# Kernel tuning notes

Measured on AMD Instinct MI355X. Metric: run time of the kernel, lower is better.

## Reference

```python
import jax, jax.numpy as jnp
import numpy as np

B, C, H, W = 16, 256, 64, 64
K = 3


def _binary_act(x):
    # forward: sign(x); backward: piecewise-polynomial STE surrogate out3
    sg = jax.lax.stop_gradient
    f32 = x.dtype
    m1 = (x < -1).astype(f32)
    m2 = (x < 0).astype(f32)
    m3 = (x < 1).astype(f32)
    out1 = -1.0 * m1 + (x * x + 2.0 * x) * (1.0 - m1)
    out2 = out1 * m2 + (-x * x + 2.0 * x) * (1.0 - m2)
    out3 = out2 * m3 + 1.0 * (1.0 - m3)
    return sg(jnp.sign(x)) - sg(out3) + out3


def _binarize_weight(w):
    # per-output-channel scale * sign(w) in forward; clipped identity STE in backward
    sg = jax.lax.stop_gradient
    scale = sg(jnp.mean(jnp.abs(w), axis=(1, 2, 3), keepdims=True))  # (O,1,1,1)
    bw_no_grad = scale * jnp.sign(w)
    cw = jnp.clip(w, -1.0, 1.0)
    return sg(bw_no_grad) - sg(cw) + cw


def setup_inputs() -> dict:
    key = jax.random.key(0)
    k1, k2 = jax.random.split(key, 2)
    x = jax.random.normal(k1, (B, C, H, W), dtype=jnp.float32)
    conv_w = jax.random.normal(k2, (C, C, K, K), dtype=jnp.float32) * 0.05
    move0_bias = jnp.zeros((1, C, 1, 1), dtype=jnp.float32)
    pr_bias0 = jnp.zeros((1, C, 1, 1), dtype=jnp.float32)
    prelu_alpha = jnp.full((C,), 0.25, dtype=jnp.float32)  # torch PReLU default
    pr_bias1 = jnp.zeros((1, C, 1, 1), dtype=jnp.float32)
    return {"x": x, "move0_bias": move0_bias, "conv_w": conv_w,
            "pr_bias0": pr_bias0, "prelu_alpha": prelu_alpha, "pr_bias1": pr_bias1}


def reference(x, move0_bias, conv_w, pr_bias0, prelu_alpha, pr_bias1):
    out = x + move0_bias                       # LearnableBias move0
    out = _binary_act(out)                     # BinaryActivation (values in {-1,0,1})
    bw = _binarize_weight(conv_w)              # HardBinaryConv weight binarization
    pad = K // 2
    out = jax.lax.conv_general_dilated(
        out, bw, window_strides=(1, 1), padding=((pad, pad), (pad, pad)),
        dimension_numbers=("NCHW", "OIHW", "NCHW"))
    # RPReLU: bias0 -> per-channel PReLU -> bias1
    out = out + pr_bias0
    a = prelu_alpha.reshape(1, -1, 1, 1)
    out = jnp.where(out >= 0, out, a * out)
    out = out + pr_bias1
    return out + x                             # residual
```

## Files before the change

kernel.cpp:

```cpp
#include <hip/hip_runtime.h>
#include <hip/hip_bf16.h>
#include <stdint.h>

#define B_ 16
#define C_ 256
#define H_ 64
#define W_ 64
#define WP 66
#define HP 66
#define ROWB (WP * 128)
#define STAGEB (3 * ROWB + 32)

typedef __attribute__((ext_vector_type(4))) float f32x4;
typedef __attribute__((ext_vector_type(4))) int int4v;
typedef __attribute__((ext_vector_type(8))) int int8v;

typedef const __attribute__((address_space(1))) uint32_t* gptr_t;
typedef __attribute__((address_space(3))) uint32_t* lptr_t;

__device__ __forceinline__ void gl_lds16(const void* g, void* l) {
  __builtin_amdgcn_global_load_lds((gptr_t)g, (lptr_t)l, 16, 0, 0);
}

__device__ __forceinline__ uint8_t sgn4(float v) {
  return v > 0.f ? (uint8_t)0x2 : (v < 0.f ? (uint8_t)0xA : (uint8_t)0);
}

#define EXT8(v4) __builtin_shufflevector((v4), (v4), 0, 1, 2, 3, -1, -1, -1, -1)

__global__ void prep_w(const float* __restrict__ w, float* __restrict__ scale,
                       uint8_t* __restrict__ wtb) {
  int o = blockIdx.x, c = threadIdx.x;
  const float* wo = w + (size_t)o * 2304 + (size_t)c * 9;
  float v[9];
  float s = 0.f;
#pragma unroll
  for (int t = 0; t < 9; ++t) { v[t] = wo[t]; s += fabsf(v[t]); }
  __shared__ float red[256];
  __shared__ uint8_t sg[9][256];
  red[c] = s;
#pragma unroll
  for (int t = 0; t < 9; ++t) sg[t][c] = sgn4(v[t]);
  __syncthreads();
  for (int st = 128; st > 0; st >>= 1) {
    if (c < st) red[c] += red[c + st];
    __syncthreads();
  }
  if (c == 0) scale[o] = red[0] / 2304.0f;
  if (c < 128) {
    int k = c;
    int ot = o >> 6, mi = (o >> 4) & 3, lm = o & 15;
    int kh = k >> 6, lk = (k >> 4) & 3, jb = k & 15;
    int l = lk * 16 + lm;
#pragma unroll
    for (int t = 0; t < 9; ++t) {
      uint8_t byte = (uint8_t)(sg[t][2 * k] | (sg[t][2 * k + 1] << 4));
      wtb[((((size_t)t * 4 + ot) * 2 + kh) * 4 + mi) * 1024 + l * 16 + jb] = byte;
    }
  }
}

__global__ void binarize(const float* __restrict__ x, const float* __restrict__ bias,
                         uint8_t* __restrict__ a_p) {
  int bh = blockIdx.x, b = bh >> 6, h = bh & 63, c0 = blockIdx.y * 64;
  int tid = threadIdx.x;
  __shared__ uint8_t lt[64][72];
#pragma unroll
  for (int p = 0; p < 4; ++p) {
    int ci = p * 16 + (tid >> 4), w4 = (tid & 15) * 4;
    f32x4 v = *(const f32x4*)(x + (((size_t)(b * C_ + c0 + ci) * H_ + h) * W_ + w4));
    float bb = bias[c0 + ci];
#pragma unroll
    for (int k = 0; k < 4; ++k) lt[w4 + k][ci] = sgn4(v[k] + bb);
  }
  __syncthreads();
  size_t rowbase = (size_t)(b * HP + h + 1) * ROWB;
#pragma unroll
  for (int r = 0; r < 2; ++r) {
    int u = r * 256 + tid;
    int w = u >> 3, q = u & 7;
    uint32_t val = 0;
#pragma unroll
    for (int e = 0; e < 8; ++e)
      val |= (uint32_t)(lt[w][q * 8 + e] & 15) << (4 * e);
    int wp = w + 1;
    int ch = (c0 + q * 8) >> 5;
    int pos = wp * 128 + (((ch ^ wp) & 7) << 4) + (q & 3) * 4;
    *(uint32_t*)(a_p + rowbase + pos) = val;
  }
  if (blockIdx.y == 0) {
    if (tid < 32) *(uint32_t*)(a_p + rowbase + tid * 4) = 0;
    else if (tid < 64) *(uint32_t*)(a_p + rowbase + 65 * 128 + (tid - 32) * 4) = 0;
  }
  if (h == 0) {
    uint32_t* zr = (uint32_t*)(a_p + (size_t)b * HP * ROWB) + blockIdx.y * 528;
    for (int k = tid; k < 528; k += 256) zr[k] = 0;
  } else if (h == 63) {
    uint32_t* zr = (uint32_t*)(a_p + ((size_t)b * HP + 65) * ROWB) + blockIdx.y * 528;
    for (int k = tid; k < 528; k += 256) zr[k] = 0;
  }
}

#define LOADW(dst, t, kh) {                                                       \
  const uint8_t* wb_ = wtb + ((((size_t)(t) * 4 + wv) * 2 + (kh)) * 4) * 1024 + l * 16; \
  _Pragma("unroll") for (int mi = 0; mi < 4; ++mi)                                \
      dst[mi] = *(const int4v*)(wb_ + mi * 1024); }

#define LOADB(dst, d, dxi, kh) {                                                  \
  int ch_ = (kh) * 4 + lk;                                                        \
  _Pragma("unroll") for (int ni = 0; ni < 4; ++ni) {                              \
    int wp_ = ni * 16 + lm + (dxi);                                               \
    dst[ni] = *(const int4v*)(smem + (d) * ROWB + wp_ * 128 +                     \
                              (((ch_ ^ wp_) & 7) << 4)); } }

#define MFMA_BURST(wreg)                                                          \
  __builtin_amdgcn_s_setprio(1);                                                  \
  _Pragma("unroll") for (int mi = 0; mi < 4; ++mi)                                \
    _Pragma("unroll") for (int ni = 0; ni < 4; ++ni)                              \
      acc[mi][ni] = __builtin_amdgcn_mfma_scale_f32_16x16x128_f8f6f4(             \
          EXT8(wreg[mi]), EXT8(bf[ni]), acc[mi][ni], 4, 4, 0, 127, 0, 127);       \
  __builtin_amdgcn_s_setprio(0);

__global__ __launch_bounds__(256, 3) void bconv(
    const uint8_t* __restrict__ a_p, const uint8_t* __restrict__ wtb,
    const float* __restrict__ scale, const float* __restrict__ x,
    const float* __restrict__ pb0, const float* __restrict__ alpha,
    const float* __restrict__ pb1, float* __restrict__ out) {
  __shared__ __attribute__((aligned(16))) uint8_t smem[STAGEB];
  int bh = (blockIdx.x & 7) * 128 + (blockIdx.x >> 3);
  int b = bh >> 6, h = bh & 63;
  int tid = threadIdx.x, l = tid & 63, wv = tid >> 6;
  int lm = l & 15, lk = l >> 4;
  int wm = wv * 64;

  const uint8_t* src = a_p + (size_t)(b * HP + h) * ROWB;
#pragma unroll
  for (int it = 0; it < 6; ++it)
    gl_lds16(src + (size_t)(it * 256 + tid) * 16, smem + it * 4096 + wv * 1024);
  if (tid < 48) gl_lds16(src + 24576 + (size_t)tid * 16, smem + 24576);

  f32x4 acc[4][4];
#pragma unroll
  for (int i = 0; i < 4; ++i)
#pragma unroll
    for (int j = 0; j < 4; ++j) acc[i][j] = (f32x4){0.f, 0.f, 0.f, 0.f};

  asm volatile("s_waitcnt vmcnt(0)" ::: "memory");
  __syncthreads();

  int4v wA[4], wB[4], bf[4];
  LOADW(wA, 0, 0)
#pragma unroll 1
  for (int t = 0; t < 9; ++t) {
    int d = t / 3, dxi = t - d * 3;
    LOADW(wB, t, 1)
    LOADB(bf, d, dxi, 0)
    MFMA_BURST(wA)
    if (t < 8) { LOADW(wA, t + 1, 0) }
    LOADB(bf, d, dxi, 1)
    MFMA_BURST(wB)
  }

  size_t xb = (size_t)b * C_ * H_ * W_ + (size_t)h * W_;
#pragma unroll
  for (int mi = 0; mi < 4; ++mi) {
#pragma unroll
    for (int j = 0; j < 4; ++j) {
      int o = wm + mi * 16 + lk * 4 + j;
      float sc = scale[o], b0 = pb0[o], al = alpha[o], b1 = pb1[o];
      size_t rowo = xb + (size_t)o * (H_ * W_);
#pragma unroll
      for (int ni = 0; ni < 4; ++ni) {
        int wcol = ni * 16 + lm;
        float v = acc[mi][ni][j] * sc + b0;
        v = v >= 0.f ? v : al * v;
        v = v + b1 + x[rowo + wcol];
        out[rowo + wcol] = v;
      }
    }
  }
}

extern "C" void kernel_launch(void* const* d_in, const int* in_sizes, int n_in,
                              void* d_out, int out_size, void* d_ws, size_t ws_size,
                              hipStream_t stream) {
  const float* x     = (const float*)d_in[0];
  const float* m0b   = (const float*)d_in[1];
  const float* w     = (const float*)d_in[2];
  const float* pb0   = (const float*)d_in[3];
  const float* alpha = (const float*)d_in[4];
  const float* pb1   = (const float*)d_in[5];
  float* out = (float*)d_out;

  float* scale = (float*)d_ws;
  uint8_t* wtb = (uint8_t*)d_ws + 4096;
  uint8_t* a_p = (uint8_t*)d_ws + 4096 + (size_t)9 * 4 * 2 * 4 * 1024 + 1024;

  hipLaunchKernelGGL(prep_w, dim3(C_), dim3(256), 0, stream, w, scale, wtb);
  hipLaunchKernelGGL(binarize, dim3(B_ * H_, C_ / 64), dim3(256), 0, stream, x, m0b, a_p);
  hipLaunchKernelGGL(bconv, dim3(B_ * H_), dim3(256), 0, stream,
                     a_p, wtb, scale, x, pb0, alpha, pb1, out);
}
```

Before: 53.92 us.

## Fuse activation binarization into conv kernel, recomputing halo rows per block

Removes the separate binarize kernel and its packed intermediate buffer. Each conv block now reads three input rows of x for all channels, binarizes them, packs them into swizzled LDS and zeroes the padding. This saves a launch and the global round trip of the packed activations. In exchange each input row is read and binarized three times, and the previously asynchronous global-to-LDS loads become synchronous staged work before the MFMA loop.

```diff
diff --git a/kernel.cpp b/kernel.cpp
--- a/kernel.cpp
+++ b/kernel.cpp
@@ -7,20 +7,12 @@
 #define H_ 64
 #define W_ 64
 #define WP 66
-#define HP 66
 #define ROWB (WP * 128)
-#define STAGEB (3 * ROWB + 32)
+#define STAGEB (3 * ROWB)
 
 typedef __attribute__((ext_vector_type(4))) float f32x4;
 typedef __attribute__((ext_vector_type(4))) int int4v;
 typedef __attribute__((ext_vector_type(8))) int int8v;
-
-typedef const __attribute__((address_space(1))) uint32_t* gptr_t;
-typedef __attribute__((address_space(3))) uint32_t* lptr_t;
-
-__device__ __forceinline__ void gl_lds16(const void* g, void* l) {
-  __builtin_amdgcn_global_load_lds((gptr_t)g, (lptr_t)l, 16, 0, 0);
-}
 
 __device__ __forceinline__ uint8_t sgn4(float v) {
   return v > 0.f ? (uint8_t)0x2 : (v < 0.f ? (uint8_t)0xA : (uint8_t)0);
@@ -60,47 +52,6 @@
   }
 }
 
-__global__ void binarize(const float* __restrict__ x, const float* __restrict__ bias,
-                         uint8_t* __restrict__ a_p) {
-  int bh = blockIdx.x, b = bh >> 6, h = bh & 63, c0 = blockIdx.y * 64;
-  int tid = threadIdx.x;
-  __shared__ uint8_t lt[64][72];
-#pragma unroll
-  for (int p = 0; p < 4; ++p) {
-    int ci = p * 16 + (tid >> 4), w4 = (tid & 15) * 4;
-    f32x4 v = *(const f32x4*)(x + (((size_t)(b * C_ + c0 + ci) * H_ + h) * W_ + w4));
-    float bb = bias[c0 + ci];
-#pragma unroll
-    for (int k = 0; k < 4; ++k) lt[w4 + k][ci] = sgn4(v[k] + bb);
-  }
-  __syncthreads();
-  size_t rowbase = (size_t)(b * HP + h + 1) * ROWB;
-#pragma unroll
-  for (int r = 0; r < 2; ++r) {
-    int u = r * 256 + tid;
-    int w = u >> 3, q = u & 7;
-    uint32_t val = 0;
-#pragma unroll
-    for (int e = 0; e < 8; ++e)
-      val |= (uint32_t)(lt[w][q * 8 + e] & 15) << (4 * e);
-    int wp = w + 1;
-    int ch = (c0 + q * 8) >> 5;
-    int pos = wp * 128 + (((ch ^ wp) & 7) << 4) + (q & 3) * 4;
-    *(uint32_t*)(a_p + rowbase + pos) = val;
-  }
-  if (blockIdx.y == 0) {
-    if (tid < 32) *(uint32_t*)(a_p + rowbase + tid * 4) = 0;
-    else if (tid < 64) *(uint32_t*)(a_p + rowbase + 65 * 128 + (tid - 32) * 4) = 0;
-  }
-  if (h == 0) {
-    uint32_t* zr = (uint32_t*)(a_p + (size_t)b * HP * ROWB) + blockIdx.y * 528;
-    for (int k = tid; k < 528; k += 256) zr[k] = 0;
-  } else if (h == 63) {
-    uint32_t* zr = (uint32_t*)(a_p + ((size_t)b * HP + 65) * ROWB) + blockIdx.y * 528;
-    for (int k = tid; k < 528; k += 256) zr[k] = 0;
-  }
-}
-
 #define LOADW(dst, t, kh) {                                                       \
   const uint8_t* wb_ = wtb + ((((size_t)(t) * 4 + wv) * 2 + (kh)) * 4) * 1024 + l * 16; \
   _Pragma("unroll") for (int mi = 0; mi < 4; ++mi)                                \
@@ -122,31 +73,62 @@
   __builtin_amdgcn_s_setprio(0);
 
 __global__ __launch_bounds__(256, 3) void bconv(
-    const uint8_t* __restrict__ a_p, const uint8_t* __restrict__ wtb,
-    const float* __restrict__ scale, const float* __restrict__ x,
+    const uint8_t* __restrict__ wtb, const float* __restrict__ scale,
+    const float* __restrict__ x, const float* __restrict__ m0b,
     const float* __restrict__ pb0, const float* __restrict__ alpha,
     const float* __restrict__ pb1, float* __restrict__ out) {
   __shared__ __attribute__((aligned(16))) uint8_t smem[STAGEB];
+  __shared__ uint8_t lt[64][268];
   int bh = (blockIdx.x & 7) * 128 + (blockIdx.x >> 3);
   int b = bh >> 6, h = bh & 63;
   int tid = threadIdx.x, l = tid & 63, wv = tid >> 6;
   int lm = l & 15, lk = l >> 4;
   int wm = wv * 64;
 
-  const uint8_t* src = a_p + (size_t)(b * HP + h) * ROWB;
+#pragma unroll 1
+  for (int r = 0; r < 3; ++r) {
+    int hr = h - 1 + r;
+    bool valid = (hr >= 0) && (hr < H_);
+    if (valid) {
 #pragma unroll
-  for (int it = 0; it < 6; ++it)
-    gl_lds16(src + (size_t)(it * 256 + tid) * 16, smem + it * 4096 + wv * 1024);
-  if (tid < 48) gl_lds16(src + 24576 + (size_t)tid * 16, smem + 24576);
+      for (int p = 0; p < 16; ++p) {
+        int ci = p * 16 + (tid >> 4), w4 = (tid & 15) * 4;
+        f32x4 v = *(const f32x4*)(x + (((size_t)(b * C_ + ci) * H_ + hr) * W_ + w4));
+        float bb = m0b[ci];
+#pragma unroll
+        for (int k = 0; k < 4; ++k) lt[w4 + k][ci] = sgn4(v[k] + bb);
+      }
+    }
+    __syncthreads();
+    int q = tid & 31;
+#pragma unroll
+    for (int rr = 0; rr < 8; ++rr) {
+      int u = rr * 256 + tid, w = u >> 5;
+      uint32_t val = 0;
+      if (valid) {
+        uint32_t a0 = *(const uint32_t*)&lt[w][q * 8];
+        uint32_t a1 = *(const uint32_t*)&lt[w][q * 8 + 4];
+        val = (a0 & 0xFu) | ((a0 >> 4) & 0xF0u) | ((a0 >> 8) & 0xF00u) |
+              ((a0 >> 12) & 0xF000u);
+        val |= ((a1 & 0xFu) | ((a1 >> 4) & 0xF0u) | ((a1 >> 8) & 0xF00u) |
+                ((a1 >> 12) & 0xF000u)) << 16;
+      }
+      int wp = w + 1;
+      *(uint32_t*)(smem + r * ROWB + wp * 128 + ((((q >> 2) ^ wp) & 7) << 4) +
+                   (q & 3) * 4) = val;
+    }
+    if (tid < 64) {
+      int px = (tid >> 5) ? 65 : 0;
+      *(uint32_t*)(smem + r * ROWB + px * 128 + (tid & 31) * 4) = 0;
+    }
+    __syncthreads();
+  }
 
   f32x4 acc[4][4];
 #pragma unroll
   for (int i = 0; i < 4; ++i)
 #pragma unroll
     for (int j = 0; j < 4; ++j) acc[i][j] = (f32x4){0.f, 0.f, 0.f, 0.f};
-
-  asm volatile("s_waitcnt vmcnt(0)" ::: "memory");
-  __syncthreads();
 
   int4v wA[4], wB[4], bf[4];
   LOADW(wA, 0, 0)
@@ -194,10 +176,8 @@
 
   float* scale = (float*)d_ws;
   uint8_t* wtb = (uint8_t*)d_ws + 4096;
-  uint8_t* a_p = (uint8_t*)d_ws + 4096 + (size_t)9 * 4 * 2 * 4 * 1024 + 1024;
 
   hipLaunchKernelGGL(prep_w, dim3(C_), dim3(256), 0, stream, w, scale, wtb);
-  hipLaunchKernelGGL(binarize, dim3(B_ * H_, C_ / 64), dim3(256), 0, stream, x, m0b, a_p);
   hipLaunchKernelGGL(bconv, dim3(B_ * H_), dim3(256), 0, stream,
-                     a_p, wtb, scale, x, pb0, alpha, pb1, out);
+                     wtb, scale, x, m0b, pb0, alpha, pb1, out);
 }
```

Result: slower. 71.11 us (+31.9%).
